# Optimization experiments

Measured on AMD Instinct MI355X. Metric: run time of the kernel, lower is better.

The kernel has to match this reference:

```python
import jax, jax.numpy as jnp
import numpy as np

B, S, H, NH, FF, L, BLK, R = 2, 4096, 768, 12, 3072, 4, 64, 3
NB = S // BLK          # 64 blocks
D = H // NH            # 64 per-head dim
A = 3 + 2 + R          # window(3) + global(2) + random(R) attended blocks
EPS = 1e-12
SCALE = 1.0 / np.sqrt(D).astype(np.float32)


def setup_inputs() -> dict:
    key = jax.random.key(0)
    ks = jax.random.split(key, 12)
    p = lambda k, shp: jax.random.normal(k, shp, jnp.float32) * 0.02
    return {
        "input_ids": jax.random.normal(ks[0], (B, S, 4), jnp.float32),
        "rand_blocks": jax.random.randint(ks[1], (NB, R), 0, NB, jnp.int32),
        "emb_w": p(ks[2], (4, H)), "emb_b": jnp.zeros((H,), jnp.float32),
        "ln1_g": jnp.ones((L, H), jnp.float32), "ln1_b": jnp.zeros((L, H), jnp.float32),
        "wq": p(ks[3], (L, H, H)), "bq": jnp.zeros((L, H), jnp.float32),
        "wk": p(ks[4], (L, H, H)), "bk": jnp.zeros((L, H), jnp.float32),
        "wv": p(ks[5], (L, H, H)), "bv": jnp.zeros((L, H), jnp.float32),
        "wo": p(ks[6], (L, H, H)), "bo": jnp.zeros((L, H), jnp.float32),
        "ln2_g": jnp.ones((L, H), jnp.float32), "ln2_b": jnp.zeros((L, H), jnp.float32),
        "w1": p(ks[7], (L, H, FF)), "b1": jnp.zeros((L, FF), jnp.float32),
        "w2": p(ks[8], (L, FF, H)), "b2": jnp.zeros((L, H), jnp.float32),
        "clf_w": p(ks[9], (H, 4)), "clf_b": jnp.zeros((4,), jnp.float32),
    }


def _ln(x, g, b):
    m = x.mean(-1, keepdims=True)
    v = jnp.var(x, axis=-1, keepdims=True)  # biased var, like torch LayerNorm
    return (x - m) * jax.lax.rsqrt(v + EPS) * g + b


def _attend_idx(rand_blocks):
    # per query block: [i-1, i, i+1] window (edge-clamped), global {0, NB-1}, R random
    ar = jnp.arange(NB)
    win = jnp.stack([jnp.clip(ar - 1, 0, NB - 1), ar, jnp.clip(ar + 1, 0, NB - 1)], 1)
    glb = jnp.broadcast_to(jnp.array([0, NB - 1], jnp.int32), (NB, 2))
    return jnp.concatenate([win.astype(jnp.int32), glb, rand_blocks], 1)  # [NB, A]


def _attn(x, wq, bq, wk, bk, wv, bv, wo, bo, idx):
    def heads(t):  # [B,S,H] -> [B,NH,NB,BLK,D]
        return t.reshape(B, NB, BLK, NH, D).transpose(0, 3, 1, 2, 4)
    q = heads(x @ wq + bq)
    k = heads(x @ wk + bk)
    v = heads(x @ wv + bv)
    kg = k[:, :, idx].reshape(B, NH, NB, A * BLK, D)  # gather attended key blocks
    vg = v[:, :, idx].reshape(B, NH, NB, A * BLK, D)
    s = jnp.einsum('bhnqd,bhnkd->bhnqk', q, kg) * SCALE  # [B,NH,NB,BLK,A*BLK]
    p = jax.nn.softmax(s, axis=-1)
    o = jnp.einsum('bhnqk,bhnkd->bhnqd', p, vg)
    o = o.transpose(0, 2, 3, 1, 4).reshape(B, S, H)
    return o @ wo + bo


def reference(input_ids, rand_blocks, emb_w, emb_b, ln1_g, ln1_b, wq, bq, wk, bk,
              wv, bv, wo, bo, ln2_g, ln2_b, w1, b1, w2, b2, clf_w, clf_b):
    idx = _attend_idx(rand_blocks)
    x = input_ids @ emb_w + emb_b
    for l in range(L):
        h = _ln(x, ln1_g[l], ln1_b[l])
        x = x + _attn(h, wq[l], bq[l], wk[l], bk[l], wv[l], bv[l], wo[l], bo[l], idx)
        h = _ln(x, ln2_g[l], ln2_b[l])
        x = x + (jax.nn.gelu(h @ w1[l] + b1[l], approximate=False) @ w2[l] + b2[l])
    logits = x @ clf_w + clf_b
    return jax.nn.softmax(logits, axis=-1)
```

## Files before the change

### kernel.cpp

```cpp
#include <hip/hip_runtime.h>
#include <math.h>

constexpr int B  = 2;
constexpr int S  = 4096;
constexpr int H  = 768;
constexpr int NH = 12;
constexpr int FF = 3072;
constexpr int L  = 4;
constexpr int R  = 3;
constexpr int NB = 64;
constexpr int AB = 8;
constexpr float SCALE = 0.125f;
constexpr int QKV_N = 3 * H;

constexpr int ROWS = B * S;
constexpr size_t XSZ = (size_t)B * S * H;

typedef short bf16x8 __attribute__((ext_vector_type(8)));
typedef unsigned short u16x8 __attribute__((ext_vector_type(8)));
typedef float f32x4 __attribute__((ext_vector_type(4)));
typedef unsigned short ushort_t;

__device__ __forceinline__ ushort_t f2b(float f) {
  union { float f; unsigned u; } c; c.f = f;
  unsigned r = c.u + 0x7fffu + ((c.u >> 16) & 1u);
  return (ushort_t)(r >> 16);
}

__device__ __forceinline__ void gload16(const void* g, void* l) {
  __builtin_amdgcn_global_load_lds(
      (const __attribute__((address_space(1))) unsigned int*)g,
      (__attribute__((address_space(3))) unsigned int*)l, 16, 0, 0);
}

__global__ __launch_bounds__(256) void embed_kernel(
    const float* __restrict__ ids, const float* __restrict__ w,
    const float* __restrict__ bvec, float* __restrict__ x) {
  int i = blockIdx.x * 256 + threadIdx.x;
  if (i >= (int)XSZ) return;
  int hc = i % H;
  int bs = i / H;
  float s = bvec[hc];
  #pragma unroll
  for (int j = 0; j < 4; ++j) s += ids[bs * 4 + j] * w[j * H + hc];
  x[i] = s;
}

__global__ __launch_bounds__(256) void ln_kernel(
    const float* __restrict__ x, const float* __restrict__ g,
    const float* __restrict__ bvec, ushort_t* __restrict__ out) {
  int row = blockIdx.x;
  const float* xr = x + (size_t)row * H;
  int t = threadIdx.x;
  float v0 = xr[t], v1 = xr[t + 256], v2 = xr[t + 512];
  float s  = v0 + v1 + v2;
  float ss = v0 * v0 + v1 * v1 + v2 * v2;
  for (int off = 1; off < 64; off <<= 1) {
    s  += __shfl_xor(s,  off);
    ss += __shfl_xor(ss, off);
  }
  __shared__ float sm[8];
  int w = t >> 6, lane = t & 63;
  if (lane == 0) { sm[w] = s; sm[4 + w] = ss; }
  __syncthreads();
  s  = sm[0] + sm[1] + sm[2] + sm[3];
  ss = sm[4] + sm[5] + sm[6] + sm[7];
  float mean = s * (1.0f / H);
  float var  = ss * (1.0f / H) - mean * mean;
  float rstd = rsqrtf(var + 1e-12f);
  ushort_t* orow = out + (size_t)row * H;
  orow[t]       = f2b((v0 - mean) * rstd * g[t]       + bvec[t]);
  orow[t + 256] = f2b((v1 - mean) * rstd * g[t + 256] + bvec[t + 256]);
  orow[t + 512] = f2b((v2 - mean) * rstd * g[t + 512] + bvec[t + 512]);
}

__global__ __launch_bounds__(256) void tcvt_kernel(
    const float* __restrict__ in, ushort_t* __restrict__ out,
    int K, int N, size_t inZ, size_t outZ) {
  __shared__ float tile[32][33];
  const float* inz = in + blockIdx.z * inZ;
  ushort_t* outz = out + blockIdx.z * outZ;
  int k0 = blockIdx.y * 32, n0 = blockIdx.x * 32;
  int tx = threadIdx.x & 31, ty = threadIdx.x >> 5;
  #pragma unroll
  for (int i = 0; i < 4; ++i) {
    int kk = ty + i * 8;
    tile[kk][tx] = inz[(size_t)(k0 + kk) * N + n0 + tx];
  }
  __syncthreads();
  #pragma unroll
  for (int i = 0; i < 4; ++i) {
    int nn = ty + i * 8;
    outz[(size_t)(n0 + nn) * K + k0 + tx] = f2b(tile[tx][nn]);
  }
}

__global__ __launch_bounds__(256) void concat_bias_kernel(
    const float* __restrict__ bq, const float* __restrict__ bk,
    const float* __restrict__ bv, float* __restrict__ out) {
  int i = blockIdx.x * 256 + threadIdx.x;
  if (i >= L * QKV_N) return;
  int l = i / QKV_N, c = i % QKV_N;
  float val = (c < H) ? bq[l * H + c] : (c < 2 * H) ? bk[l * H + c - H] : bv[l * H + c - 2 * H];
  out[i] = val;
}

template <int EPI>
__global__ __launch_bounds__(256, 3) void bgemm(
    const ushort_t* __restrict__ A, const ushort_t* __restrict__ Wt,
    const float* __restrict__ bias, const float* __restrict__ res,
    float* __restrict__ Cf, ushort_t* __restrict__ Cb,
    int M, int N, int K, int ncol) {
  constexpr int LDSB = 8192;
  __shared__ ushort_t lds[3 * LDSB];

  const int nwg = (int)gridDim.x;
  const int qq = nwg >> 3, r0 = nwg & 7;
  const int xcd = (int)blockIdx.x & 7, loc = (int)blockIdx.x >> 3;
  const int swz = (xcd < r0 ? xcd * (qq + 1) : r0 * (qq + 1) + (xcd - r0) * qq) + loc;
  const int bm = (swz / ncol) * 128, bn = (swz % ncol) * 128;

  const int t = threadIdx.x;
  const int wid = t >> 6, lane = t & 63;
  const int fcol = lane & 15, fgrp = lane >> 4;
  const int wm = wid >> 1, wn = wid & 1;

  const ushort_t* src[4];
  int dst[4];
  #pragma unroll
  for (int j = 0; j < 4; ++j) {
    int idx = j * 2048 + t * 8;
    dst[j] = idx;
    int ch = (idx >> 3) & 3;
    int row;
    const ushort_t* base;
    if (idx < 4096) { row = idx >> 5;           base = A  + (size_t)(bm + row) * K; }
    else            { row = (idx - 4096) >> 5;  base = Wt + (size_t)(bn + row) * K; }
    src[j] = base + ((ch ^ ((row >> 1) & 3)) << 3);
  }

  f32x4 acc[4][4] = {};

  #pragma unroll
  for (int j = 0; j < 4; ++j) gload16(src[j], &lds[dst[j]]);
  #pragma unroll
  for (int j = 0; j < 4; ++j) gload16(src[j] + 32, &lds[LDSB + dst[j]]);
  int kgl = 64;

  int bo0 = 0, bo1 = LDSB, bo2 = 2 * LDSB;
  const int NT = K >> 5;
  for (int tau = 0; tau < NT; ++tau) {
    if (tau + 2 < NT) {
      #pragma unroll
      for (int j = 0; j < 4; ++j) gload16(src[j] + kgl, &lds[bo2 + dst[j]]);
      kgl += 32;
      asm volatile("s_waitcnt vmcnt(8)" ::: "memory");
    } else if (tau + 2 == NT) {
      asm volatile("s_waitcnt vmcnt(4)" ::: "memory");
    } else {
      asm volatile("s_waitcnt vmcnt(0)" ::: "memory");
    }
    __builtin_amdgcn_sched_barrier(0);
    __builtin_amdgcn_s_barrier();
    __builtin_amdgcn_sched_barrier(0);

    bf16x8 af[4], bfr[4];
    #pragma unroll
    for (int mi = 0; mi < 4; ++mi) {
      int row = wm * 64 + mi * 16 + fcol;
      af[mi] = *(const bf16x8*)&lds[bo0 + row * 32 + ((fgrp ^ ((row >> 1) & 3)) << 3)];
    }
    #pragma unroll
    for (int ni = 0; ni < 4; ++ni) {
      int row = wn * 64 + ni * 16 + fcol;
      bfr[ni] = *(const bf16x8*)&lds[bo0 + 4096 + row * 32 + ((fgrp ^ ((row >> 1) & 3)) << 3)];
    }
    __builtin_amdgcn_s_setprio(1);
    #pragma unroll
    for (int mi = 0; mi < 4; ++mi)
      #pragma unroll
      for (int ni = 0; ni < 4; ++ni)
        acc[mi][ni] = __builtin_amdgcn_mfma_f32_16x16x32_bf16(af[mi], bfr[ni], acc[mi][ni], 0, 0, 0);
    __builtin_amdgcn_s_setprio(0);

    if (tau < NT - 1) {
      __builtin_amdgcn_sched_barrier(0);
      __builtin_amdgcn_s_barrier();
      __builtin_amdgcn_sched_barrier(0);
    }
    int tmp = bo0; bo0 = bo1; bo1 = bo2; bo2 = tmp;
  }

  #pragma unroll
  for (int mi = 0; mi < 4; ++mi) {
    const int m = bm + wm * 64 + mi * 16 + fgrp * 4;
    #pragma unroll
    for (int ni = 0; ni < 4; ++ni) {
      const int n = bn + wn * 64 + ni * 16 + fcol;
      const float bb = bias[n];
      #pragma unroll
      for (int r = 0; r < 4; ++r) {
        float val = acc[mi][ni][r] + bb;
        if (EPI == 1) {
          Cf[(size_t)(m + r) * N + n] = val + res[(size_t)(m + r) * N + n];
        } else if (EPI == 2) {
          val = 0.5f * val * (1.0f + erff(val * 0.70710678118654752f));
          Cb[(size_t)(m + r) * N + n] = f2b(val);
        } else {
          Cb[(size_t)(m + r) * N + n] = f2b(val);
        }
      }
    }
  }
}

__global__ __launch_bounds__(256) void attn_mfma(
    const ushort_t* __restrict__ qkv, const int* __restrict__ rb,
    ushort_t* __restrict__ ao) {
  __shared__ ushort_t Ks[64 * 72];
  __shared__ ushort_t Vt[64 * 72];
  __shared__ ushort_t Ps[4][16 * 72];
  const int n = blockIdx.x, hh = blockIdx.y, b = blockIdx.z;
  const int t = threadIdx.x;
  const int wid = t >> 6, lane = t & 63;
  const int fcol = lane & 15, fgrp = lane >> 4;
  const int qr0 = n * 64 + wid * 16;

  bf16x8 qf[2];
  #pragma unroll
  for (int kc = 0; kc < 2; ++kc)
    qf[kc] = *(const bf16x8*)&qkv[((size_t)(b * S) + qr0 + fcol) * QKV_N + hh * 64 + kc * 32 + fgrp * 8];

  f32x4 oacc[4] = {};
  float mrow[4], lrow[4];
  #pragma unroll
  for (int r = 0; r < 4; ++r) { mrow[r] = -1e30f; lrow[r] = 0.f; }

  const int skp = t >> 3;
  const int sdo = (t & 7) * 8;

  for (int a = 0; a < AB; ++a) {
    int kb;
    if      (a == 0) kb = (n > 0) ? n - 1 : 0;
    else if (a == 1) kb = n;
    else if (a == 2) kb = (n < NB - 1) ? n + 1 : NB - 1;
    else if (a == 3) kb = 0;
    else if (a == 4) kb = NB - 1;
    else             kb = rb[n * R + (a - 5)];

    const ushort_t* kbase = qkv + ((size_t)(b * S) + kb * 64) * QKV_N + H + hh * 64;
    const ushort_t* vbase = qkv + ((size_t)(b * S) + kb * 64) * QKV_N + 2 * H + hh * 64;
    #pragma unroll
    for (int i = 0; i < 2; ++i) {
      int kp = skp + i * 32;
      u16x8 kv = *(const u16x8*)&kbase[(size_t)kp * QKV_N + sdo];
      *(u16x8*)&Ks[kp * 72 + sdo] = kv;
      u16x8 vv = *(const u16x8*)&vbase[(size_t)kp * QKV_N + sdo];
      #pragma unroll
      for (int j = 0; j < 8; ++j) Vt[(sdo + j) * 72 + kp] = vv[j];
    }
    __syncthreads();

    f32x4 sacc[4] = {};
    #pragma unroll
    for (int ni = 0; ni < 4; ++ni)
      #pragma unroll
      for (int kc = 0; kc < 2; ++kc) {
        bf16x8 kf = *(const bf16x8*)&Ks[(ni * 16 + fcol) * 72 + kc * 32 + fgrp * 8];
        sacc[ni] = __builtin_amdgcn_mfma_f32_16x16x32_bf16(qf[kc], kf, sacc[ni], 0, 0, 0);
      }

    #pragma unroll
    for (int ni = 0; ni < 4; ++ni)
      #pragma unroll
      for (int r = 0; r < 4; ++r) sacc[ni][r] *= SCALE;
    #pragma unroll
    for (int r = 0; r < 4; ++r) {
      float tm = fmaxf(fmaxf(sacc[0][r], sacc[1][r]), fmaxf(sacc[2][r], sacc[3][r]));
      tm = fmaxf(tm, __shfl_xor(tm, 1));
      tm = fmaxf(tm, __shfl_xor(tm, 2));
      tm = fmaxf(tm, __shfl_xor(tm, 4));
      tm = fmaxf(tm, __shfl_xor(tm, 8));
      float mn = fmaxf(mrow[r], tm);
      float corr = __expf(mrow[r] - mn);
      mrow[r] = mn;
      float rs = 0.f;
      #pragma unroll
      for (int ni = 0; ni < 4; ++ni) {
        float p = __expf(sacc[ni][r] - mn);
        sacc[ni][r] = p;
        rs += p;
      }
      rs += __shfl_xor(rs, 1);
      rs += __shfl_xor(rs, 2);
      rs += __shfl_xor(rs, 4);
      rs += __shfl_xor(rs, 8);
      lrow[r] = lrow[r] * corr + rs;
      #pragma unroll
      for (int ni = 0; ni < 4; ++ni) oacc[ni][r] *= corr;
    }

    __syncthreads();
    #pragma unroll
    for (int ni = 0; ni < 4; ++ni)
      #pragma unroll
      for (int r = 0; r < 4; ++r)
        Ps[wid][(fgrp * 4 + r) * 72 + ni * 16 + fcol] = f2b(sacc[ni][r]);
    __syncthreads();

    #pragma unroll
    for (int kc = 0; kc < 2; ++kc) {
      bf16x8 pa = *(const bf16x8*)&Ps[wid][fcol * 72 + kc * 32 + fgrp * 8];
      #pragma unroll
      for (int ni = 0; ni < 4; ++ni) {
        bf16x8 vb = *(const bf16x8*)&Vt[(ni * 16 + fcol) * 72 + kc * 32 + fgrp * 8];
        oacc[ni] = __builtin_amdgcn_mfma_f32_16x16x32_bf16(pa, vb, oacc[ni], 0, 0, 0);
      }
    }
    __syncthreads();
  }

  #pragma unroll
  for (int r = 0; r < 4; ++r) {
    float inv = 1.0f / lrow[r];
    int row = qr0 + fgrp * 4 + r;
    #pragma unroll
    for (int ni = 0; ni < 4; ++ni)
      ao[((size_t)(b * S) + row) * H + hh * 64 + ni * 16 + fcol] = f2b(oacc[ni][r] * inv);
  }
}

__global__ __launch_bounds__(64) void clf_kernel(
    const float* __restrict__ x, const float* __restrict__ w,
    const float* __restrict__ bvec, float* __restrict__ out) {
  int row = blockIdx.x;
  int lane = threadIdx.x;
  const float* xr = x + (size_t)row * H;
  float p0 = 0.f, p1 = 0.f, p2 = 0.f, p3 = 0.f;
  for (int d = lane; d < H; d += 64) {
    float xv = xr[d];
    p0 += xv * w[d * 4 + 0];
    p1 += xv * w[d * 4 + 1];
    p2 += xv * w[d * 4 + 2];
    p3 += xv * w[d * 4 + 3];
  }
  for (int off = 1; off < 64; off <<= 1) {
    p0 += __shfl_xor(p0, off);
    p1 += __shfl_xor(p1, off);
    p2 += __shfl_xor(p2, off);
    p3 += __shfl_xor(p3, off);
  }
  if (lane == 0) {
    float l0 = p0 + bvec[0], l1 = p1 + bvec[1], l2 = p2 + bvec[2], l3 = p3 + bvec[3];
    float mx = fmaxf(fmaxf(l0, l1), fmaxf(l2, l3));
    float e0 = __expf(l0 - mx), e1 = __expf(l1 - mx), e2 = __expf(l2 - mx), e3 = __expf(l3 - mx);
    float inv = 1.0f / (e0 + e1 + e2 + e3);
    out[row * 4 + 0] = e0 * inv;
    out[row * 4 + 1] = e1 * inv;
    out[row * 4 + 2] = e2 * inv;
    out[row * 4 + 3] = e3 * inv;
  }
}

extern "C" void kernel_launch(void* const* d_in, const int* in_sizes, int n_in,
                              void* d_out, int out_size, void* d_ws, size_t ws_size,
                              hipStream_t stream) {
  const float* input_ids = (const float*)d_in[0];
  const int*   rand_bl   = (const int*)  d_in[1];
  const float* emb_w = (const float*)d_in[2];
  const float* emb_b = (const float*)d_in[3];
  const float* ln1_g = (const float*)d_in[4];
  const float* ln1_b = (const float*)d_in[5];
  const float* wq = (const float*)d_in[6];
  const float* bq = (const float*)d_in[7];
  const float* wk = (const float*)d_in[8];
  const float* bk = (const float*)d_in[9];
  const float* wv = (const float*)d_in[10];
  const float* bv = (const float*)d_in[11];
  const float* wo = (const float*)d_in[12];
  const float* bo = (const float*)d_in[13];
  const float* ln2_g = (const float*)d_in[14];
  const float* ln2_b = (const float*)d_in[15];
  const float* w1 = (const float*)d_in[16];
  const float* b1 = (const float*)d_in[17];
  const float* w2 = (const float*)d_in[18];
  const float* b2 = (const float*)d_in[19];
  const float* clf_w = (const float*)d_in[20];
  const float* clf_b = (const float*)d_in[21];

  char* p = (char*)d_ws;
  float*    x    = (float*)p;    p += XSZ * 4;
  ushort_t* h    = (ushort_t*)p; p += XSZ * 2;
  ushort_t* qkv  = (ushort_t*)p; p += (size_t)ROWS * QKV_N * 2;
  ushort_t* ao   = (ushort_t*)p; p += XSZ * 2;
  ushort_t* ff   = qkv;
  ushort_t* qkvT = (ushort_t*)p; p += (size_t)L * QKV_N * H * 2;
  ushort_t* woT  = (ushort_t*)p; p += (size_t)L * H * H * 2;
  ushort_t* w1T  = (ushort_t*)p; p += (size_t)L * H * FF * 2;
  ushort_t* w2T  = (ushort_t*)p; p += (size_t)L * FF * H * 2;
  float*    bqkv = (float*)p;    p += (size_t)L * QKV_N * 4;

  tcvt_kernel<<<dim3(H / 32, H / 32, L), 256, 0, stream>>>(
      wq, qkvT + 0 * H * H, H, H, (size_t)H * H, (size_t)QKV_N * H);
  tcvt_kernel<<<dim3(H / 32, H / 32, L), 256, 0, stream>>>(
      wk, qkvT + 1 * H * H, H, H, (size_t)H * H, (size_t)QKV_N * H);
  tcvt_kernel<<<dim3(H / 32, H / 32, L), 256, 0, stream>>>(
      wv, qkvT + 2 * H * H, H, H, (size_t)H * H, (size_t)QKV_N * H);
  tcvt_kernel<<<dim3(H / 32, H / 32, L), 256, 0, stream>>>(
      wo, woT, H, H, (size_t)H * H, (size_t)H * H);
  tcvt_kernel<<<dim3(FF / 32, H / 32, L), 256, 0, stream>>>(
      w1, w1T, H, FF, (size_t)H * FF, (size_t)H * FF);
  tcvt_kernel<<<dim3(H / 32, FF / 32, L), 256, 0, stream>>>(
      w2, w2T, FF, H, (size_t)FF * H, (size_t)FF * H);
  concat_bias_kernel<<<(L * QKV_N + 255) / 256, 256, 0, stream>>>(bq, bk, bv, bqkv);

  embed_kernel<<<(int)((XSZ + 255) / 256), 256, 0, stream>>>(input_ids, emb_w, emb_b, x);

  for (int l = 0; l < L; ++l) {
    ln_kernel<<<ROWS, 256, 0, stream>>>(x, ln1_g + l * H, ln1_b + l * H, h);

    bgemm<0><<<(ROWS / 128) * (QKV_N / 128), 256, 0, stream>>>(
        h, qkvT + (size_t)l * QKV_N * H, bqkv + l * QKV_N, nullptr,
        nullptr, qkv, ROWS, QKV_N, H, QKV_N / 128);

    attn_mfma<<<dim3(NB, NH, B), 256, 0, stream>>>(qkv, rand_bl, ao);

    bgemm<1><<<(ROWS / 128) * (H / 128), 256, 0, stream>>>(
        ao, woT + (size_t)l * H * H, bo + l * H, x, x, nullptr, ROWS, H, H, H / 128);

    ln_kernel<<<ROWS, 256, 0, stream>>>(x, ln2_g + l * H, ln2_b + l * H, h);

    bgemm<2><<<(ROWS / 128) * (FF / 128), 256, 0, stream>>>(
        h, w1T + (size_t)l * H * FF, b1 + l * FF, nullptr,
        nullptr, ff, ROWS, FF, H, FF / 128);

    bgemm<1><<<(ROWS / 128) * (H / 128), 256, 0, stream>>>(
        ff, w2T + (size_t)l * FF * H, b2 + l * H, x, x, nullptr, ROWS, H, FF, H / 128);
  }

  clf_kernel<<<ROWS, 64, 0, stream>>>(x, clf_w, clf_b, (float*)d_out);
}
```

Baseline: 1.075 ms.

## Write V transposed from QKV GEMM and load attention operands directly to registers

The QKV GEMM epilogue now writes the V columns into a separate transposed buffer (head-dim major, token minor) instead of the row-major qkv buffer. The attention kernel then loads K and V fragments straight from global memory into registers, dropping the LDS staging, the scalar LDS transpose of V and most block-wide barriers. Only the per-wave P buffer remains in LDS, and MFMA sections get raised priority. The cost is uncoalesced-ish fragment loads from global and strided 8-byte transposed stores in the GEMM epilogue.

```diff
diff --git a/kernel.cpp b/kernel.cpp
--- a/kernel.cpp
+++ b/kernel.cpp
@@ -18,6 +18,7 @@
 
 typedef short bf16x8 __attribute__((ext_vector_type(8)));
 typedef unsigned short u16x8 __attribute__((ext_vector_type(8)));
+typedef unsigned short u16x4 __attribute__((ext_vector_type(4)));
 typedef float f32x4 __attribute__((ext_vector_type(4)));
 typedef unsigned short ushort_t;
 
@@ -109,7 +110,7 @@
 __global__ __launch_bounds__(256, 3) void bgemm(
     const ushort_t* __restrict__ A, const ushort_t* __restrict__ Wt,
     const float* __restrict__ bias, const float* __restrict__ res,
-    float* __restrict__ Cf, ushort_t* __restrict__ Cb,
+    float* __restrict__ Cf, ushort_t* __restrict__ Cb, ushort_t* __restrict__ Cv,
     int M, int N, int K, int ncol) {
   constexpr int LDSB = 8192;
   __shared__ ushort_t lds[3 * LDSB];
@@ -191,6 +192,22 @@
     int tmp = bo0; bo0 = bo1; bo1 = bo2; bo2 = tmp;
   }
 
+  if (EPI == 0 && bn >= 2 * H) {
+    #pragma unroll
+    for (int mi = 0; mi < 4; ++mi) {
+      const int m = bm + wm * 64 + mi * 16 + fgrp * 4;
+      #pragma unroll
+      for (int ni = 0; ni < 4; ++ni) {
+        const int n = bn + wn * 64 + ni * 16 + fcol;
+        const float bb = bias[n];
+        u16x4 pk;
+        #pragma unroll
+        for (int r = 0; r < 4; ++r) pk[r] = f2b(acc[mi][ni][r] + bb);
+        *(u16x4*)&Cv[(size_t)(n - 2 * H) * M + m] = pk;
+      }
+    }
+    return;
+  }
   #pragma unroll
   for (int mi = 0; mi < 4; ++mi) {
     const int m = bm + wm * 64 + mi * 16 + fgrp * 4;
@@ -215,10 +232,8 @@
 }
 
 __global__ __launch_bounds__(256) void attn_mfma(
-    const ushort_t* __restrict__ qkv, const int* __restrict__ rb,
-    ushort_t* __restrict__ ao) {
-  __shared__ ushort_t Ks[64 * 72];
-  __shared__ ushort_t Vt[64 * 72];
+    const ushort_t* __restrict__ qkv, const ushort_t* __restrict__ vT,
+    const int* __restrict__ rb, ushort_t* __restrict__ ao) {
   __shared__ ushort_t Ps[4][16 * 72];
   const int n = blockIdx.x, hh = blockIdx.y, b = blockIdx.z;
   const int t = threadIdx.x;
@@ -236,39 +251,46 @@
   #pragma unroll
   for (int r = 0; r < 4; ++r) { mrow[r] = -1e30f; lrow[r] = 0.f; }
 
-  const int skp = t >> 3;
-  const int sdo = (t & 7) * 8;
+  int kbs[AB];
+  kbs[0] = (n > 0) ? n - 1 : 0;
+  kbs[1] = n;
+  kbs[2] = (n < NB - 1) ? n + 1 : NB - 1;
+  kbs[3] = 0;
+  kbs[4] = NB - 1;
+  kbs[5] = rb[n * R + 0];
+  kbs[6] = rb[n * R + 1];
+  kbs[7] = rb[n * R + 2];
+
+  const ushort_t* kbaseH = qkv + (size_t)(b * S) * QKV_N + H + hh * 64;
+  const ushort_t* vbaseH = vT + (size_t)(hh * 64) * ROWS + b * S;
 
   for (int a = 0; a < AB; ++a) {
-    int kb;
-    if      (a == 0) kb = (n > 0) ? n - 1 : 0;
-    else if (a == 1) kb = n;
-    else if (a == 2) kb = (n < NB - 1) ? n + 1 : NB - 1;
-    else if (a == 3) kb = 0;
-    else if (a == 4) kb = NB - 1;
-    else             kb = rb[n * R + (a - 5)];
-
-    const ushort_t* kbase = qkv + ((size_t)(b * S) + kb * 64) * QKV_N + H + hh * 64;
-    const ushort_t* vbase = qkv + ((size_t)(b * S) + kb * 64) * QKV_N + 2 * H + hh * 64;
-    #pragma unroll
-    for (int i = 0; i < 2; ++i) {
-      int kp = skp + i * 32;
-      u16x8 kv = *(const u16x8*)&kbase[(size_t)kp * QKV_N + sdo];
-      *(u16x8*)&Ks[kp * 72 + sdo] = kv;
-      u16x8 vv = *(const u16x8*)&vbase[(size_t)kp * QKV_N + sdo];
-      #pragma unroll
-      for (int j = 0; j < 8; ++j) Vt[(sdo + j) * 72 + kp] = vv[j];
-    }
-    __syncthreads();
+    const int kb = kbs[a];
+
+    bf16x8 kf[4][2];
+    #pragma unroll
+    for (int ni = 0; ni < 4; ++ni)
+      #pragma unroll
+      for (int kc = 0; kc < 2; ++kc)
+        kf[ni][kc] = *(const bf16x8*)&kbaseH[
+            (size_t)(kb * 64 + ni * 16 + fcol) * QKV_N + kc * 32 + fgrp * 8];
 
     f32x4 sacc[4] = {};
-    #pragma unroll
-    for (int ni = 0; ni < 4; ++ni)
-      #pragma unroll
-      for (int kc = 0; kc < 2; ++kc) {
-        bf16x8 kf = *(const bf16x8*)&Ks[(ni * 16 + fcol) * 72 + kc * 32 + fgrp * 8];
-        sacc[ni] = __builtin_amdgcn_mfma_f32_16x16x32_bf16(qf[kc], kf, sacc[ni], 0, 0, 0);
-      }
+    __builtin_amdgcn_s_setprio(1);
+    #pragma unroll
+    for (int ni = 0; ni < 4; ++ni)
+      #pragma unroll
+      for (int kc = 0; kc < 2; ++kc)
+        sacc[ni] = __builtin_amdgcn_mfma_f32_16x16x32_bf16(qf[kc], kf[ni][kc], sacc[ni], 0, 0, 0);
+    __builtin_amdgcn_s_setprio(0);
+
+    bf16x8 vb[4][2];
+    #pragma unroll
+    for (int ni = 0; ni < 4; ++ni)
+      #pragma unroll
+      for (int kc = 0; kc < 2; ++kc)
+        vb[ni][kc] = *(const bf16x8*)&vbaseH[
+            (size_t)(ni * 16 + fcol) * ROWS + kb * 64 + kc * 32 + fgrp * 8];
 
     #pragma unroll
     for (int ni = 0; ni < 4; ++ni)
@@ -300,24 +322,24 @@
       for (int ni = 0; ni < 4; ++ni) oacc[ni][r] *= corr;
     }
 
-    __syncthreads();
     #pragma unroll
     for (int ni = 0; ni < 4; ++ni)
       #pragma unroll
       for (int r = 0; r < 4; ++r)
         Ps[wid][(fgrp * 4 + r) * 72 + ni * 16 + fcol] = f2b(sacc[ni][r]);
-    __syncthreads();
-
-    #pragma unroll
-    for (int kc = 0; kc < 2; ++kc) {
-      bf16x8 pa = *(const bf16x8*)&Ps[wid][fcol * 72 + kc * 32 + fgrp * 8];
-      #pragma unroll
-      for (int ni = 0; ni < 4; ++ni) {
-        bf16x8 vb = *(const bf16x8*)&Vt[(ni * 16 + fcol) * 72 + kc * 32 + fgrp * 8];
-        oacc[ni] = __builtin_amdgcn_mfma_f32_16x16x32_bf16(pa, vb, oacc[ni], 0, 0, 0);
-      }
-    }
-    __syncthreads();
+
+    bf16x8 pa[2];
+    #pragma unroll
+    for (int kc = 0; kc < 2; ++kc)
+      pa[kc] = *(const bf16x8*)&Ps[wid][fcol * 72 + kc * 32 + fgrp * 8];
+
+    __builtin_amdgcn_s_setprio(1);
+    #pragma unroll
+    for (int kc = 0; kc < 2; ++kc)
+      #pragma unroll
+      for (int ni = 0; ni < 4; ++ni)
+        oacc[ni] = __builtin_amdgcn_mfma_f32_16x16x32_bf16(pa[kc], vb[ni][kc], oacc[ni], 0, 0, 0);
+    __builtin_amdgcn_s_setprio(0);
   }
 
   #pragma unroll
@@ -394,6 +416,7 @@
   ushort_t* qkv  = (ushort_t*)p; p += (size_t)ROWS * QKV_N * 2;
   ushort_t* ao   = (ushort_t*)p; p += XSZ * 2;
   ushort_t* ff   = qkv;
+  ushort_t* vT   = (ushort_t*)p; p += (size_t)H * ROWS * 2;
   ushort_t* qkvT = (ushort_t*)p; p += (size_t)L * QKV_N * H * 2;
   ushort_t* woT  = (ushort_t*)p; p += (size_t)L * H * H * 2;
   ushort_t* w1T  = (ushort_t*)p; p += (size_t)L * H * FF * 2;
@@ -421,21 +444,21 @@
 
     bgemm<0><<<(ROWS / 128) * (QKV_N / 128), 256, 0, stream>>>(
         h, qkvT + (size_t)l * QKV_N * H, bqkv + l * QKV_N, nullptr,
-        nullptr, qkv, ROWS, QKV_N, H, QKV_N / 128);
-
-    attn_mfma<<<dim3(NB, NH, B), 256, 0, stream>>>(qkv, rand_bl, ao);
+        nullptr, qkv, vT, ROWS, QKV_N, H, QKV_N / 128);
+
+    attn_mfma<<<dim3(NB, NH, B), 256, 0, stream>>>(qkv, vT, rand_bl, ao);
 
     bgemm<1><<<(ROWS / 128) * (H / 128), 256, 0, stream>>>(
-        ao, woT + (size_t)l * H * H, bo + l * H, x, x, nullptr, ROWS, H, H, H / 128);
+        ao, woT + (size_t)l * H * H, bo + l * H, x, x, nullptr, nullptr, ROWS, H, H, H / 128);
 
     ln_kernel<<<ROWS, 256, 0, stream>>>(x, ln2_g + l * H, ln2_b + l * H, h);
 
     bgemm<2><<<(ROWS / 128) * (FF / 128), 256, 0, stream>>>(
         h, w1T + (size_t)l * H * FF, b1 + l * FF, nullptr,
-        nullptr, ff, ROWS, FF, H, FF / 128);
+        nullptr, ff, nullptr, ROWS, FF, H, FF / 128);
 
     bgemm<1><<<(ROWS / 128) * (H / 128), 256, 0, stream>>>(
-        ff, w2T + (size_t)l * FF * H, b2 + l * H, x, x, nullptr, ROWS, H, FF, H / 128);
+        ff, w2T + (size_t)l * FF * H, b2 + l * H, x, x, nullptr, nullptr, ROWS, H, FF, H / 128);
   }
 
   clf_kernel<<<ROWS, 64, 0, stream>>>(x, clf_w, clf_b, (float*)d_out);
```

After: 1.176 ms. 9.4% more time.
